# Optimization experiments

Hardware: AMD Instinct MI355X
Metric: run time of the kernel (lower is better)

## Reference

```python
import jax, jax.numpy as jnp
import numpy as np

CHANNEL = 512
INTER = CHANNEL // 2


def setup_inputs() -> dict:
    key = jax.random.key(0)
    ks = jax.random.split(key, 7)
    b, c, h, w = 8, CHANNEL, 64, 64
    q = jax.random.normal(ks[0], (b, c, h, w), dtype=jnp.float32)
    k = jax.random.normal(ks[1], (b, c, h, w), dtype=jnp.float32)
    v = jax.random.normal(ks[2], (b, c, h, w), dtype=jnp.float32)
    # 1x1 conv weights, no bias: (out_ch, in_ch)
    s_in = 1.0 / np.sqrt(c)
    s_int = 1.0 / np.sqrt(INTER)
    W_phi = jax.random.uniform(ks[3], (INTER, c), jnp.float32, -s_in, s_in)
    W_theta = jax.random.uniform(ks[4], (INTER, c), jnp.float32, -s_in, s_in)
    W_g = jax.random.uniform(ks[5], (INTER, c), jnp.float32, -s_in, s_in)
    W_mask = jax.random.uniform(ks[6], (c, INTER), jnp.float32, -s_int, s_int)
    return {"q": q, "k": k, "v": v, "W_phi": W_phi, "W_theta": W_theta,
            "W_g": W_g, "W_mask": W_mask}


def reference(q, k, v, W_phi, W_theta, W_g, W_mask):
    b, c, h, w = q.shape
    inter = c // 2
    hw2 = (h * w) // 2  # quirk: conv output (b, c/2, h, w) is reshaped to (b, c, hw/2)
    # 1x1 convs as channel matmuls
    phi = jnp.einsum('oc,bchw->bohw', W_phi, q).reshape(b, c, hw2)        # (b, c, hw2)
    theta = jnp.einsum('oc,bchw->bohw', W_theta, k).reshape(b, c, hw2)    # (b, c, hw2)
    g = jnp.einsum('oc,bchw->bohw', W_g, v).reshape(b, c, hw2)            # (b, c, hw2)
    # scores: (b, hw2, c) @ (b, c, hw2) -> (b, hw2, hw2)
    scores = jnp.einsum('bcn,bcm->bnm', theta, phi)
    attn = jax.nn.softmax(scores, axis=1)  # torch Softmax(dim=1): over rows
    # (b, hw2, hw2) @ (b, hw2, c) -> (b, hw2, c)
    y = jnp.einsum('bnm,bcn->bmc', attn, g)
    y = jnp.transpose(y, (0, 2, 1)).reshape(b, inter, h, w)
    mask = jnp.einsum('oc,bchw->bohw', W_mask, y)
    return mask + q + v
```

## Files before the change

kernel.cpp:

```cpp
#include <hip/hip_runtime.h>
#include <hip/hip_bf16.h>
#include <math.h>

typedef __hip_bfloat16 hbf16;
typedef __attribute__((ext_vector_type(8))) short short8;
typedef __attribute__((ext_vector_type(4))) float f32x4;

static const long QS = 2097152;

__device__ __forceinline__ unsigned short f2bf(float f) {
    hbf16 h = __float2bfloat16(f);
    return *reinterpret_cast<unsigned short*>(&h);
}
__device__ __forceinline__ float bf2f(unsigned short u) {
    unsigned x = ((unsigned)u) << 16;
    return __uint_as_float(x);
}
__device__ __forceinline__ unsigned pk2(float a, float b) {
    return (unsigned)f2bf(a) | ((unsigned)f2bf(b) << 16);
}

__device__ __forceinline__ void gload16(const void* g, void* l) {
    __builtin_amdgcn_global_load_lds(
        (const __attribute__((address_space(1))) void*)g,
        (__attribute__((address_space(3))) void*)l, 16, 0, 0);
}

template <bool PTM, bool DUAL>
__global__ __launch_bounds__(256) void convmm(
    const float* __restrict__ X0, const float* __restrict__ X1,
    const short* __restrict__ W, long selW,
    short* __restrict__ C, long selC,
    int ldc, long bsX, long bsC)
{
    __shared__ __align__(16) float Lf[32 * 256];
    __shared__ __align__(16) short Ps[256 * 40];
    __shared__ __align__(16) short Ws[64 * 40];

    const int tid = threadIdx.x;
    const int w = tid >> 6, lane = tid & 63;
    const int quad = lane >> 4, l16 = lane & 15;

    int bz = blockIdx.z, sel = 0;
    if constexpr (DUAL) { sel = bz & 1; bz >>= 1; }

    const int p0 = (PTM ? blockIdx.y : blockIdx.x) * 256;
    const int w0 = (PTM ? blockIdx.x : blockIdx.y) * 64;

    const float* X = ((DUAL && sel) ? X1 : X0) + (long)bz * bsX;
    const short* Wp = W + (long)sel * selW;
    short* Cp = C + (long)bz * bsC + (long)sel * selC;

    const int wr = tid >> 2, wc = tid & 3;
    short8 wreg;

    f32x4 acc[4][4];
#pragma unroll
    for (int i = 0; i < 4; ++i)
#pragma unroll
        for (int j = 0; j < 4; ++j) acc[i][j] = (f32x4){0.f, 0.f, 0.f, 0.f};

    auto issueX = [&](int k0) {
#pragma unroll
        for (int i = 0; i < 8; ++i) {
            int e = i * 1024 + tid * 4;
            int kc = e >> 8, p = e & 255;
            gload16(X + (long)(k0 + kc) * 4096 + p0 + p,
                    Lf + i * 1024 + w * 256);
        }
    };
    auto loadW = [&](int k0) {
        wreg = *reinterpret_cast<const short8*>(
            &Wp[(long)(w0 + wr) * 512 + k0 + wc * 8]);
    };

    issueX(0);
    loadW(0);

    for (int k0 = 0; k0 < 512; k0 += 32) {
        __syncthreads();

#pragma unroll
        for (int u = 0; u < 4; ++u) {
            float f[8];
#pragma unroll
            for (int j = 0; j < 8; ++j) f[j] = Lf[(u * 8 + j) * 256 + tid];
            uint4 pk;
            pk.x = pk2(f[0], f[1]);
            pk.y = pk2(f[2], f[3]);
            pk.z = pk2(f[4], f[5]);
            pk.w = pk2(f[6], f[7]);
            *reinterpret_cast<uint4*>(&Ps[tid * 40 + u * 8]) = pk;
        }
        *reinterpret_cast<short8*>(&Ws[wr * 40 + wc * 8]) = wreg;

        __syncthreads();

        if (k0 + 32 < 512) { issueX(k0 + 32); loadW(k0 + 32); }

        short8 af[4], bf[4];
#pragma unroll
        for (int mt = 0; mt < 4; ++mt) {
            int r = PTM ? (w * 64 + mt * 16 + l16) : (mt * 16 + l16);
            const short* base = PTM ? Ps : Ws;
            af[mt] = *reinterpret_cast<const short8*>(&base[r * 40 + quad * 8]);
        }
#pragma unroll
        for (int nt = 0; nt < 4; ++nt) {
            int r = PTM ? (nt * 16 + l16) : (w * 64 + nt * 16 + l16);
            const short* base = PTM ? Ws : Ps;
            bf[nt] = *reinterpret_cast<const short8*>(&base[r * 40 + quad * 8]);
        }
#pragma unroll
        for (int mt = 0; mt < 4; ++mt)
#pragma unroll
            for (int nt = 0; nt < 4; ++nt)
                acc[mt][nt] = __builtin_amdgcn_mfma_f32_16x16x32_bf16(
                    af[mt], bf[nt], acc[mt][nt], 0, 0, 0);
    }

#pragma unroll
    for (int mt = 0; mt < 4; ++mt)
#pragma unroll
        for (int nt = 0; nt < 4; ++nt)
#pragma unroll
            for (int reg = 0; reg < 4; ++reg) {
                int gr = (PTM ? (blockIdx.y * 256 + w * 64 + mt * 16)
                              : (blockIdx.y * 64 + mt * 16)) + quad * 4 + reg;
                int gc = (PTM ? (blockIdx.x * 64 + nt * 16)
                              : (blockIdx.x * 256 + w * 64 + nt * 16)) + l16;
                Cp[(long)gr * ldc + gc] = (short)f2bf(acc[mt][nt][reg]);
            }
}

template <int R>
__device__ __forceinline__ void stage_direct(const short* P, int ld, int row0,
                                             long koff, short* Ls) {
    const int tid = threadIdx.x;
    const int w = tid >> 6, lane = tid & 63;
    const int lrow = lane >> 3;
    const int s = lane & 7;
#pragma unroll
    for (int j = 0; j < R / 32; ++j) {
        int rowbase = w * (R / 4) + j * 8;
        int r = rowbase + lrow;
        int g = s ^ (r & 7);
        const short* ga = P + (long)(row0 + r) * ld + koff + g * 8;
        gload16(ga, Ls + rowbase * 64);
    }
}

#define EPI_BF 0
#define EPI_YT 1
#define EPI_OUT 2

template <int TM, int TN, int EPI>
__global__ __launch_bounds__(256) void mm(
    const short* __restrict__ A, const short* __restrict__ B,
    void* __restrict__ C, const float* __restrict__ Rq, const float* __restrict__ Rv,
    int K, int lda, int ldb, int ldc, int kmask, int kshift, long kpanel,
    long bsA, long bsB, long bsC, long bsR)
{
    __shared__ __align__(16) short As[TM * 64];
    __shared__ __align__(16) short Bs[TN * 64];

    const int tid = threadIdx.x;
    const int w = tid >> 6, lane = tid & 63;
    const int quad = lane >> 4, l16 = lane & 15;
    const int m0 = blockIdx.y * TM;
    const int n0 = blockIdx.x * TN;
    const int bz = blockIdx.z;

    A += (long)bz * bsA;
    B += (long)bz * bsB;
    const long cb = (long)bz * bsC;
    if constexpr (EPI == EPI_OUT) { Rq += (long)bz * bsR; Rv += (long)bz * bsR; }

    constexpr int WM = TM / 2;
    constexpr int MT = WM / 16;
    const int wm = (w & 1) * WM;
    const int wn = (w >> 1) * 64;

    f32x4 acc[MT][4];
#pragma unroll
    for (int i = 0; i < MT; ++i)
#pragma unroll
        for (int j = 0; j < 4; ++j) acc[i][j] = (f32x4){0.f, 0.f, 0.f, 0.f};

    for (int k0 = 0; k0 < K; k0 += 64) {
        __syncthreads();
        long koff = (long)(k0 & kmask) + (long)(k0 >> kshift) * kpanel;
        stage_direct<TM>(A, lda, m0, koff, As);
        stage_direct<TN>(B, ldb, n0, koff, Bs);
        __syncthreads();

#pragma unroll
        for (int ks = 0; ks < 2; ++ks) {
            short8 af[MT], bfr[4];
#pragma unroll
            for (int mt = 0; mt < MT; ++mt) {
                int r = wm + mt * 16 + l16;
                int s = (ks * 4 + quad) ^ (r & 7);
                af[mt] = *reinterpret_cast<const short8*>(&As[r * 64 + s * 8]);
            }
#pragma unroll
            for (int nt = 0; nt < 4; ++nt) {
                int r = wn + nt * 16 + l16;
                int s = (ks * 4 + quad) ^ (r & 7);
                bfr[nt] = *reinterpret_cast<const short8*>(&Bs[r * 64 + s * 8]);
            }
#pragma unroll
            for (int mt = 0; mt < MT; ++mt)
#pragma unroll
                for (int nt = 0; nt < 4; ++nt)
                    acc[mt][nt] = __builtin_amdgcn_mfma_f32_16x16x32_bf16(
                        af[mt], bfr[nt], acc[mt][nt], 0, 0, 0);
        }
    }

#pragma unroll
    for (int mt = 0; mt < MT; ++mt)
#pragma unroll
        for (int nt = 0; nt < 4; ++nt)
#pragma unroll
            for (int reg = 0; reg < 4; ++reg) {
                int gr = m0 + wm + mt * 16 + quad * 4 + reg;
                int gc = n0 + wn + nt * 16 + l16;
                float vacc = acc[mt][nt][reg];
                if constexpr (EPI == EPI_BF) {
                    ((short*)C)[cb + (long)gr * ldc + gc] = (short)f2bf(vacc);
                } else if constexpr (EPI == EPI_YT) {
                    long a = (long)gc * 256 + (long)(gr & 1) * 524288 + (gr >> 1);
                    ((short*)C)[cb + a] = (short)f2bf(vacc);
                } else {
                    long a = (long)gr * 4096 + gc;
                    ((float*)C)[cb + a] = vacc + Rq[a] + Rv[a];
                }
            }
}

__global__ __launch_bounds__(256) void softmax_row(short* __restrict__ T) {
    const int row = blockIdx.x;
    const int tid = threadIdx.x;
    const int w = tid >> 6, lane = tid & 63;
    __shared__ float red[8];

    uint4 u = *reinterpret_cast<const uint4*>(&T[(long)row * 2048 + tid * 8]);
    float f[8];
    f[0] = bf2f((unsigned short)(u.x & 0xffff)); f[1] = bf2f((unsigned short)(u.x >> 16));
    f[2] = bf2f((unsigned short)(u.y & 0xffff)); f[3] = bf2f((unsigned short)(u.y >> 16));
    f[4] = bf2f((unsigned short)(u.z & 0xffff)); f[5] = bf2f((unsigned short)(u.z >> 16));
    f[6] = bf2f((unsigned short)(u.w & 0xffff)); f[7] = bf2f((unsigned short)(u.w >> 16));

    float m = f[0];
#pragma unroll
    for (int j = 1; j < 8; ++j) m = fmaxf(m, f[j]);
    for (int o = 32; o > 0; o >>= 1) m = fmaxf(m, __shfl_down(m, o));
    if (lane == 0) red[w] = m;
    __syncthreads();
    float M = fmaxf(fmaxf(red[0], red[1]), fmaxf(red[2], red[3]));

    float e[8], s = 0.f;
#pragma unroll
    for (int j = 0; j < 8; ++j) { e[j] = __expf(f[j] - M); s += e[j]; }
    for (int o = 32; o > 0; o >>= 1) s += __shfl_down(s, o);
    if (lane == 0) red[4 + w] = s;
    __syncthreads();
    float invL = 1.0f / (red[4] + red[5] + red[6] + red[7]);

    uint4 ov;
    ov.x = pk2(e[0] * invL, e[1] * invL);
    ov.y = pk2(e[2] * invL, e[3] * invL);
    ov.z = pk2(e[4] * invL, e[5] * invL);
    ov.w = pk2(e[6] * invL, e[7] * invL);
    *reinterpret_cast<uint4*>(&T[(long)row * 2048 + tid * 8]) = ov;
}

__global__ __launch_bounds__(256) void cast_w(
    const float* __restrict__ a, const float* __restrict__ b,
    const float* __restrict__ c, const float* __restrict__ d,
    short* __restrict__ W)
{
    const float* S[4] = {a, b, c, d};
    int sel = blockIdx.y;
    int i = (blockIdx.x * 256 + threadIdx.x) * 4;
    float4 f = *reinterpret_cast<const float4*>(&S[sel][i]);
    uint2 o;
    o.x = pk2(f.x, f.y);
    o.y = pk2(f.z, f.w);
    *reinterpret_cast<uint2*>(&W[sel * 131072 + i]) = o;
}

extern "C" void kernel_launch(void* const* d_in, const int* in_sizes, int n_in,
                              void* d_out, int out_size, void* d_ws, size_t ws_size,
                              hipStream_t stream)
{
    const float* q    = (const float*)d_in[0];
    const float* kk   = (const float*)d_in[1];
    const float* v    = (const float*)d_in[2];
    const float* Wphi = (const float*)d_in[3];
    const float* Wth  = (const float*)d_in[4];
    const float* Wg   = (const float*)d_in[5];
    const float* Wm   = (const float*)d_in[6];
    float* out = (float*)d_out;
    dim3 blk(256);

    const long PB = 8388608;
    long ws_shorts = (long)(ws_size / 2);
    int NB = (int)((ws_shorts - 524288) / PB);
    if (NB > 8) NB = 8;
    if (NB < 1) NB = 1;

    short* Wb   = (short*)d_ws;
    short* Phi  = Wb + 524288;
    short* Th   = Phi + (long)NB * 1048576;
    short* Gr   = Th + (long)NB * 1048576;
    short* T    = Gr + (long)NB * 1048576;
    short* YtvT = T + (long)NB * 4194304;
    const short* WbPhi = Wb;
    const short* WbG   = Wb + 262144;
    const short* WbM   = Wb + 393216;

    const int LIN_M = 0x3FFFFFFF, LIN_S = 30;

    cast_w<<<dim3(128, 4), blk, 0, stream>>>(Wphi, Wth, Wg, Wm, Wb);

    for (int b0 = 0; b0 < 8; b0 += NB) {
        int nb = 8 - b0 < NB ? 8 - b0 : NB;
        const float* qb = q + (long)b0 * QS;
        const float* kb = kk + (long)b0 * QS;
        const float* vb = v + (long)b0 * QS;

        convmm<true, true><<<dim3(4, 16, nb * 2), blk, 0, stream>>>(
            qb, kb, WbPhi, 131072, Phi, (long)NB * 1048576,
            256, QS, 1048576);

        convmm<false, false><<<dim3(16, 4, nb), blk, 0, stream>>>(
            vb, nullptr, WbG, 0, Gr, 0,
            4096, QS, 1048576);

        mm<128, 128, EPI_BF><<<dim3(16, 16, nb), blk, 0, stream>>>(
            Phi, Th, T, nullptr, nullptr,
            512, 256, 256, 2048, 255, 8, 524288,
            1048576, 1048576, 4194304, 0);

        softmax_row<<<dim3(2048 * nb), blk, 0, stream>>>(T);

        mm<64, 128, EPI_YT><<<dim3(16, 8, nb), blk, 0, stream>>>(
            Gr, T, YtvT, nullptr, nullptr,
            2048, 2048, 2048, 256, LIN_M, LIN_S, 0,
            1048576, 4194304, 1048576, 0);

        mm<128, 128, EPI_OUT><<<dim3(32, 4, nb), blk, 0, stream>>>(
            WbM, YtvT, out + (long)b0 * QS, qb, vb,
            256, 256, 256, 4096, LIN_M, LIN_S, 0,
            0, 1048576, QS, QS);
    }
}
```

Baseline: 450.5 us.

## Merge three projection convs into one 512-thread kernel with full-N tiles

Replaces the two convmm launches (phi/theta and g) with a single kernel that processes q, k and v in one grid of 512-thread blocks. Each block covers 256 pixels by all 256 output channels, so each fp32 input element is read and converted to bf16 once instead of once per 64-channel output tile. Weight fragments now go straight from global memory into registers, and the bf16 pixel tile uses an XOR-swizzled shared layout. The g output is written transposed with packed stores. The mm launches also get their grids remapped so batch index varies fastest, which changes block scheduling and L2 locality, at the cost of more register pressure in the larger conv tile.

```diff
diff --git a/kernel.cpp b/kernel.cpp
--- a/kernel.cpp
+++ b/kernel.cpp
@@ -26,52 +26,50 @@
         (__attribute__((address_space(3))) void*)l, 16, 0, 0);
 }
 
-template <bool PTM, bool DUAL>
-__global__ __launch_bounds__(256) void convmm(
-    const float* __restrict__ X0, const float* __restrict__ X1,
-    const short* __restrict__ W, long selW,
-    short* __restrict__ C, long selC,
-    int ldc, long bsX, long bsC)
+__global__ __launch_bounds__(512, 2) void convmm(
+    const float* __restrict__ Xq, const float* __restrict__ Xk,
+    const float* __restrict__ Xv,
+    const short* __restrict__ Wb,
+    short* __restrict__ Phi, long selStride,
+    short* __restrict__ Gr)
 {
     __shared__ __align__(16) float Lf[32 * 256];
-    __shared__ __align__(16) short Ps[256 * 40];
-    __shared__ __align__(16) short Ws[64 * 40];
+    __shared__ __align__(16) short Ps[128 * 64];
 
     const int tid = threadIdx.x;
     const int w = tid >> 6, lane = tid & 63;
     const int quad = lane >> 4, l16 = lane & 15;
-
-    int bz = blockIdx.z, sel = 0;
-    if constexpr (DUAL) { sel = bz & 1; bz >>= 1; }
-
-    const int p0 = (PTM ? blockIdx.y : blockIdx.x) * 256;
-    const int w0 = (PTM ? blockIdx.x : blockIdx.y) * 64;
-
-    const float* X = ((DUAL && sel) ? X1 : X0) + (long)bz * bsX;
-    const short* Wp = W + (long)sel * selW;
-    short* Cp = C + (long)bz * bsC + (long)sel * selC;
-
-    const int wr = tid >> 2, wc = tid & 3;
-    short8 wreg;
-
-    f32x4 acc[4][4];
-#pragma unroll
-    for (int i = 0; i < 4; ++i)
+    const int p0 = blockIdx.x * 256;
+    const int sel = blockIdx.z % 3;
+    const int bz = blockIdx.z / 3;
+
+    const float* X = (sel == 0 ? Xq : sel == 1 ? Xk : Xv) + (long)bz * QS;
+    const short* Wp = Wb + sel * 131072;
+
+    const int wp = (w & 1) * 128;
+    const int wo = (w >> 1) * 64;
+    const int tp = tid & 255;
+    const int kh = tid >> 8;
+
+    f32x4 acc[8][4];
+#pragma unroll
+    for (int i = 0; i < 8; ++i)
 #pragma unroll
         for (int j = 0; j < 4; ++j) acc[i][j] = (f32x4){0.f, 0.f, 0.f, 0.f};
 
     auto issueX = [&](int k0) {
 #pragma unroll
-        for (int i = 0; i < 8; ++i) {
-            int e = i * 1024 + tid * 4;
-            int kc = e >> 8, p = e & 255;
-            gload16(X + (long)(k0 + kc) * 4096 + p0 + p,
-                    Lf + i * 1024 + w * 256);
+        for (int i = 0; i < 4; ++i) {
+            int r = i * 8 + w;
+            gload16(X + (long)(k0 + r) * 4096 + p0 + lane * 4, Lf + r * 256);
         }
     };
+    short8 bfn[4];
     auto loadW = [&](int k0) {
-        wreg = *reinterpret_cast<const short8*>(
-            &Wp[(long)(w0 + wr) * 512 + k0 + wc * 8]);
+#pragma unroll
+        for (int nt = 0; nt < 4; ++nt)
+            bfn[nt] = *reinterpret_cast<const short8*>(
+                &Wp[(long)(wo + nt * 16 + l16) * 512 + k0 + quad * 8]);
     };
 
     issueX(0);
@@ -80,57 +78,74 @@
     for (int k0 = 0; k0 < 512; k0 += 32) {
         __syncthreads();
 
-#pragma unroll
-        for (int u = 0; u < 4; ++u) {
-            float f[8];
-#pragma unroll
-            for (int j = 0; j < 8; ++j) f[j] = Lf[(u * 8 + j) * 256 + tid];
-            uint4 pk;
-            pk.x = pk2(f[0], f[1]);
-            pk.y = pk2(f[2], f[3]);
-            pk.z = pk2(f[4], f[5]);
-            pk.w = pk2(f[6], f[7]);
-            *reinterpret_cast<uint4*>(&Ps[tid * 40 + u * 8]) = pk;
+        float f[16];
+#pragma unroll
+        for (int j = 0; j < 16; ++j) f[j] = Lf[(kh * 16 + j) * 256 + tp];
+        {
+            int R = tp >> 1, h = tp & 1;
+#pragma unroll
+            for (int u = 0; u < 2; ++u) {
+                uint4 pk;
+                pk.x = pk2(f[u * 8 + 0], f[u * 8 + 1]);
+                pk.y = pk2(f[u * 8 + 2], f[u * 8 + 3]);
+                pk.z = pk2(f[u * 8 + 4], f[u * 8 + 5]);
+                pk.w = pk2(f[u * 8 + 6], f[u * 8 + 7]);
+                int c = kh * 2 + u;
+                int s = (h * 4 + c) ^ (R & 7);
+                *reinterpret_cast<uint4*>(&Ps[R * 64 + s * 8]) = pk;
+            }
         }
-        *reinterpret_cast<short8*>(&Ws[wr * 40 + wc * 8]) = wreg;
+
+        short8 bcur[4];
+#pragma unroll
+        for (int nt = 0; nt < 4; ++nt) bcur[nt] = bfn[nt];
 
         __syncthreads();
 
         if (k0 + 32 < 512) { issueX(k0 + 32); loadW(k0 + 32); }
 
-        short8 af[4], bf[4];
-#pragma unroll
-        for (int mt = 0; mt < 4; ++mt) {
-            int r = PTM ? (w * 64 + mt * 16 + l16) : (mt * 16 + l16);
-            const short* base = PTM ? Ps : Ws;
-            af[mt] = *reinterpret_cast<const short8*>(&base[r * 40 + quad * 8]);
+        short8 af[8];
+#pragma unroll
+        for (int mt = 0; mt < 8; ++mt) {
+            int r = wp + mt * 16 + l16;
+            int R = r >> 1;
+            int s = ((r & 1) * 4 + quad) ^ (R & 7);
+            af[mt] = *reinterpret_cast<const short8*>(&Ps[R * 64 + s * 8]);
         }
 #pragma unroll
-        for (int nt = 0; nt < 4; ++nt) {
-            int r = PTM ? (nt * 16 + l16) : (w * 64 + nt * 16 + l16);
-            const short* base = PTM ? Ws : Ps;
-            bf[nt] = *reinterpret_cast<const short8*>(&base[r * 40 + quad * 8]);
-        }
-#pragma unroll
-        for (int mt = 0; mt < 4; ++mt)
+        for (int mt = 0; mt < 8; ++mt)
 #pragma unroll
             for (int nt = 0; nt < 4; ++nt)
                 acc[mt][nt] = __builtin_amdgcn_mfma_f32_16x16x32_bf16(
-                    af[mt], bf[nt], acc[mt][nt], 0, 0, 0);
-    }
-
-#pragma unroll
-    for (int mt = 0; mt < 4; ++mt)
-#pragma unroll
-        for (int nt = 0; nt < 4; ++nt)
-#pragma unroll
-            for (int reg = 0; reg < 4; ++reg) {
-                int gr = (PTM ? (blockIdx.y * 256 + w * 64 + mt * 16)
-                              : (blockIdx.y * 64 + mt * 16)) + quad * 4 + reg;
-                int gc = (PTM ? (blockIdx.x * 64 + nt * 16)
-                              : (blockIdx.x * 256 + w * 64 + nt * 16)) + l16;
-                Cp[(long)gr * ldc + gc] = (short)f2bf(acc[mt][nt][reg]);
-            }
+                    af[mt], bcur[nt], acc[mt][nt], 0, 0, 0);
+    }
+
+    if (sel < 2) {
+        short* Cp = Phi + (long)sel * selStride + (long)bz * 1048576;
+#pragma unroll
+        for (int mt = 0; mt < 8; ++mt)
+#pragma unroll
+            for (int nt = 0; nt < 4; ++nt)
+#pragma unroll
+                for (int reg = 0; reg < 4; ++reg) {
+                    int gr = p0 + wp + mt * 16 + quad * 4 + reg;
+                    int gc = wo + nt * 16 + l16;
+                    Cp[(long)gr * 256 + gc] = (short)f2bf(acc[mt][nt][reg]);
+                }
+    } else {
+        short* Cp = Gr + (long)bz * 1048576;
+#pragma unroll
+        for (int mt = 0; mt < 8; ++mt)
+#pragma unroll
+            for (int nt = 0; nt < 4; ++nt) {
+                int gr = p0 + wp + mt * 16 + quad * 4;
+                int gc = wo + nt * 16 + l16;
+                uint2 pk;
+                pk.x = pk2(acc[mt][nt][0], acc[mt][nt][1]);
+                pk.y = pk2(acc[mt][nt][2], acc[mt][nt][3]);
+                *reinterpret_cast<uint2*>(&Cp[(long)gc * 4096 + gr]) = pk;
+            }
+    }
 }
 
 template <int R>
@@ -154,7 +169,7 @@
 #define EPI_YT 1
 #define EPI_OUT 2
 
-template <int TM, int TN, int EPI>
+template <int TM, int TN, int EPI, int XM>
 __global__ __launch_bounds__(256) void mm(
     const short* __restrict__ A, const short* __restrict__ B,
     void* __restrict__ C, const float* __restrict__ Rq, const float* __restrict__ Rv,
@@ -167,9 +182,15 @@
     const int tid = threadIdx.x;
     const int w = tid >> 6, lane = tid & 63;
     const int quad = lane >> 4, l16 = lane & 15;
-    const int m0 = blockIdx.y * TM;
-    const int n0 = blockIdx.x * TN;
-    const int bz = blockIdx.z;
+
+    int m0, n0, bz;
+    if constexpr (XM == 0) {
+        m0 = blockIdx.y * TM; n0 = blockIdx.x * TN; bz = blockIdx.z;
+    } else if constexpr (XM == 1) {
+        bz = blockIdx.x; m0 = (blockIdx.y >> 4) * TM; n0 = (blockIdx.y & 15) * TN;
+    } else {
+        bz = blockIdx.x >> 4; n0 = (blockIdx.x & 15) * TN; m0 = blockIdx.y * TM;
+    }
 
     A += (long)bz * bsA;
     B += (long)bz * bsB;
@@ -317,9 +338,7 @@
     short* Gr   = Th + (long)NB * 1048576;
     short* T    = Gr + (long)NB * 1048576;
     short* YtvT = T + (long)NB * 4194304;
-    const short* WbPhi = Wb;
-    const short* WbG   = Wb + 262144;
-    const short* WbM   = Wb + 393216;
+    const short* WbM = Wb + 393216;
 
     const int LIN_M = 0x3FFFFFFF, LIN_S = 30;
 
@@ -331,27 +350,22 @@
         const float* kb = kk + (long)b0 * QS;
         const float* vb = v + (long)b0 * QS;
 
-        convmm<true, true><<<dim3(4, 16, nb * 2), blk, 0, stream>>>(
-            qb, kb, WbPhi, 131072, Phi, (long)NB * 1048576,
-            256, QS, 1048576);
-
-        convmm<false, false><<<dim3(16, 4, nb), blk, 0, stream>>>(
-            vb, nullptr, WbG, 0, Gr, 0,
-            4096, QS, 1048576);
-
-        mm<128, 128, EPI_BF><<<dim3(16, 16, nb), blk, 0, stream>>>(
+        convmm<<<dim3(16, 1, nb * 3), dim3(512), 0, stream>>>(
+            qb, kb, vb, Wb, Phi, (long)NB * 1048576, Gr);
+
+        mm<128, 128, EPI_BF, 1><<<dim3(nb, 256), blk, 0, stream>>>(
             Phi, Th, T, nullptr, nullptr,
             512, 256, 256, 2048, 255, 8, 524288,
             1048576, 1048576, 4194304, 0);
 
         softmax_row<<<dim3(2048 * nb), blk, 0, stream>>>(T);
 
-        mm<64, 128, EPI_YT><<<dim3(16, 8, nb), blk, 0, stream>>>(
+        mm<64, 128, EPI_YT, 2><<<dim3(16 * nb, 8), blk, 0, stream>>>(
             Gr, T, YtvT, nullptr, nullptr,
             2048, 2048, 2048, 256, LIN_M, LIN_S, 0,
             1048576, 4194304, 1048576, 0);
 
-        mm<128, 128, EPI_OUT><<<dim3(32, 4, nb), blk, 0, stream>>>(
+        mm<128, 128, EPI_OUT, 0><<<dim3(32, 4, nb), blk, 0, stream>>>(
             WbM, YtvT, out + (long)b0 * QS, qb, vb,
             256, 256, 256, 4096, LIN_M, LIN_S, 0,
             0, 1048576, QS, QS);
```

After: 419.6 us. -6.9%, faster.
